# Kernel optimization log

Hardware: AMD Instinct MI355X
Metric: run time of the kernel (lower is better)

Reference implementation:

```python
import jax, jax.numpy as jnp
import numpy as np

N_CELLTYPE = 50
M_PER_CT = 2000     # features per celltype
N_FEATURE = 20000
N_CELL = 512


def setup_inputs() -> dict:
    key = jax.random.key(0)
    k1, k2, k3 = jax.random.split(key, 3)
    x = jax.random.normal(k1, (N_FEATURE, N_CELL), dtype=jnp.float32)
    # nn.init.normal_(w, 1.0, 0.1)
    weight = 1.0 + 0.1 * jax.random.normal(k2, (N_CELLTYPE,), dtype=jnp.float32)
    idx = jax.random.randint(k3, (N_CELLTYPE, M_PER_CT), 0, N_FEATURE, dtype=jnp.int64)
    return {"x": x, "weight": weight, "idx": idx}


def reference(x, weight, idx):
    # Fused equivalent of: for each celltype ii, gather x[idx[ii]] * weight[ii],
    # vstack all, then flatten(transpose(.)).
    n_ct, m = idx.shape
    z = x[idx.reshape(-1)] * jnp.repeat(weight, m)[:, None]  # [n_ct*m, n_cell]
    return z.T.reshape(-1)  # flatten(t(z)), row-major over transposed matrix
```

## Files before the change

### kernel.cpp

```cpp
#include <hip/hip_runtime.h>

#define N_CELLTYPE 50
#define M_PER_CT   2000
#define N_FEATURE  20000
#define N_CELL     512
#define R_TOTAL    (N_CELLTYPE * M_PER_CT)
#define TR         32
#define TC         256
#define NTHREADS   512

typedef float vfloat4 __attribute__((ext_vector_type(4)));

__global__ __launch_bounds__(NTHREADS) void ct_scale_transpose(
    const float* __restrict__ x, const float* __restrict__ w,
    const int* __restrict__ idx, float* __restrict__ out) {
  __shared__ float tile[TR][TC + 4];
  __shared__ int   srow[TR];
  __shared__ float sw[TR];

  const int r0 = blockIdx.x * TR;
  const int c0 = blockIdx.y * TC;
  const int t  = threadIdx.x;

  if (t < TR) {
    const int r = r0 + t;
    srow[t] = idx[r];
    sw[t]   = w[r / M_PER_CT];
  }
  __syncthreads();

#pragma unroll
  for (int i = 0; i < 4; ++i) {
    const int linear = i * NTHREADS + t;
    const int row = linear >> 6;
    const int q   = linear & 63;
    const float4 v = *reinterpret_cast<const float4*>(
        x + (long)srow[row] * N_CELL + c0 + q * 4);
    const float s = sw[row];
    float4 sv;
    sv.x = v.x * s; sv.y = v.y * s; sv.z = v.z * s; sv.w = v.w * s;
    *reinterpret_cast<float4*>(&tile[row][q * 4]) = sv;
  }
  __syncthreads();

#pragma unroll
  for (int i = 0; i < 4; ++i) {
    const int linear = i * NTHREADS + t;
    const int c  = linear >> 3;
    const int q  = linear & 7;
    const int rr = q * 4;
    vfloat4 v;
    v.x = tile[rr + 0][c];
    v.y = tile[rr + 1][c];
    v.z = tile[rr + 2][c];
    v.w = tile[rr + 3][c];
    __builtin_nontemporal_store(
        v, reinterpret_cast<vfloat4*>(out + (long)(c0 + c) * R_TOTAL + r0 + rr));
  }
}

extern "C" void kernel_launch(void* const* d_in, const int* in_sizes, int n_in,
                              void* d_out, int out_size, void* d_ws, size_t ws_size,
                              hipStream_t stream) {
  const float* x   = (const float*)d_in[0];
  const float* w   = (const float*)d_in[1];
  const int*   idx = (const int*)d_in[2];
  float*       out = (float*)d_out;

  dim3 grid(R_TOTAL / TR, N_CELL / TC);
  ct_scale_transpose<<<grid, NTHREADS, 0, stream>>>(x, w, idx, out);
}
```

Before: 246.7 us.

## Process full gathered rows per block with swizzled LDS tile and batched loads

Each block now covers all 512 columns for its 32 gathered rows, so the grid drops to one dimension and each idx and weight lookup is used once. The padded shared tile becomes an XOR-free rotational swizzle to avoid bank conflicts on both the row-wise writes and the column-wise reads. All eight global loads are issued before any LDS store to raise memory-level parallelism. The cost is a 64KB LDS tile and more registers per thread, which can lower occupancy.

```diff
diff --git a/kernel.cpp b/kernel.cpp
--- a/kernel.cpp
+++ b/kernel.cpp
@@ -6,7 +6,7 @@
 #define N_CELL     512
 #define R_TOTAL    (N_CELLTYPE * M_PER_CT)
 #define TR         32
-#define TC         256
+#define TC         512
 #define NTHREADS   512
 
 typedef float vfloat4 __attribute__((ext_vector_type(4)));
@@ -14,12 +14,11 @@
 __global__ __launch_bounds__(NTHREADS) void ct_scale_transpose(
     const float* __restrict__ x, const float* __restrict__ w,
     const int* __restrict__ idx, float* __restrict__ out) {
-  __shared__ float tile[TR][TC + 4];
+  __shared__ float tile[TR][TC];
   __shared__ int   srow[TR];
   __shared__ float sw[TR];
 
   const int r0 = blockIdx.x * TR;
-  const int c0 = blockIdx.y * TC;
   const int t  = threadIdx.x;
 
   if (t < TR) {
@@ -29,33 +28,43 @@
   }
   __syncthreads();
 
+  float4 vv[8];
 #pragma unroll
-  for (int i = 0; i < 4; ++i) {
+  for (int i = 0; i < 8; ++i) {
     const int linear = i * NTHREADS + t;
-    const int row = linear >> 6;
-    const int q   = linear & 63;
-    const float4 v = *reinterpret_cast<const float4*>(
-        x + (long)srow[row] * N_CELL + c0 + q * 4);
+    const int row = linear >> 7;
+    const int q   = linear & 127;
+    vv[i] = *reinterpret_cast<const float4*>(
+        x + (long)srow[row] * N_CELL + q * 4);
+  }
+#pragma unroll
+  for (int i = 0; i < 8; ++i) {
+    const int linear = i * NTHREADS + t;
+    const int row = linear >> 7;
+    const int q   = linear & 127;
     const float s = sw[row];
-    float4 sv;
-    sv.x = v.x * s; sv.y = v.y * s; sv.z = v.z * s; sv.w = v.w * s;
-    *reinterpret_cast<float4*>(&tile[row][q * 4]) = sv;
+    vfloat4 sv;
+    sv.x = vv[i].x * s; sv.y = vv[i].y * s;
+    sv.z = vv[i].z * s; sv.w = vv[i].w * s;
+    const int p4 = (q + (row >> 2)) & 127;
+    *reinterpret_cast<vfloat4*>(&tile[row][p4 * 4]) = sv;
   }
   __syncthreads();
 
 #pragma unroll
-  for (int i = 0; i < 4; ++i) {
+  for (int i = 0; i < 8; ++i) {
     const int linear = i * NTHREADS + t;
     const int c  = linear >> 3;
     const int q  = linear & 7;
-    const int rr = q * 4;
+    const int p4 = ((c >> 2) + q) & 127;
+    const int e  = p4 * 4 + (c & 3);
     vfloat4 v;
-    v.x = tile[rr + 0][c];
-    v.y = tile[rr + 1][c];
-    v.z = tile[rr + 2][c];
-    v.w = tile[rr + 3][c];
+    v.x = tile[4 * q + 0][e];
+    v.y = tile[4 * q + 1][e];
+    v.z = tile[4 * q + 2][e];
+    v.w = tile[4 * q + 3][e];
     __builtin_nontemporal_store(
-        v, reinterpret_cast<vfloat4*>(out + (long)(c0 + c) * R_TOTAL + r0 + rr));
+        v, reinterpret_cast<vfloat4*>(out + (long)c * R_TOTAL + r0 + 4 * q));
   }
 }
 
@@ -67,6 +76,5 @@
   const int*   idx = (const int*)d_in[2];
   float*       out = (float*)d_out;
 
-  dim3 grid(R_TOTAL / TR, N_CELL / TC);
-  ct_scale_transpose<<<grid, NTHREADS, 0, stream>>>(x, w, idx, out);
+  ct_scale_transpose<<<dim3(R_TOTAL / TR), NTHREADS, 0, stream>>>(x, w, idx, out);
 }
```

New measurement: 247.3 us. No clear change (+0.3%).
